# Performance work log

Hardware: AMD Instinct MI355X
Metric: run time of the kernel (lower is better)

Reference implementation:

```python
import jax, jax.numpy as jnp
import numpy as np

NU = 500000   # num_users
NI = 500000   # num_items
E = 128       # embedding_dim
F = 172       # feature_dim
B = 65536     # number of events in the batch
MSG = 2 * E + F  # GRU input dim = 428


def _gru_cell(x, h, wih, whh, bih, bhh):
    # PyTorch GRUCell: gates ordered (r, z, n)
    gi = x @ wih.T + bih            # [B, 3E]
    gh = h @ whh.T + bhh            # [B, 3E]
    ir, iz, in_ = jnp.split(gi, 3, axis=-1)
    hr, hz, hn = jnp.split(gh, 3, axis=-1)
    r = jax.nn.sigmoid(ir + hr)
    z = jax.nn.sigmoid(iz + hz)
    n = jnp.tanh(in_ + r * hn)
    return (1.0 - z) * n + z * h


def setup_inputs() -> dict:
    key = jax.random.key(0)
    ks = jax.random.split(key, 18)
    s = 0.05  # init scale ~ 1/sqrt(E)
    return {
        "user_ids": jax.random.randint(ks[0], (B,), 0, NU),
        "item_ids": jax.random.randint(ks[1], (B,), 0, NI),
        "timestamps": jax.random.uniform(ks[2], (B,), dtype=jnp.float32) * 1000.0,
        "features": jax.random.normal(ks[3], (B, F), dtype=jnp.float32),
        "query_time": 1200,
        "memory": jax.random.normal(ks[4], (NU + NI, E), dtype=jnp.float32) * 0.1,
        "last_time": jax.random.uniform(ks[5], (NU + NI,), dtype=jnp.float32) * 1000.0,
        "time_w": jax.random.normal(ks[6], (E,), dtype=jnp.float32) * 0.01,  # Linear(1,E,bias=False)
        "u_wih": jax.random.normal(ks[7], (3 * E, MSG), dtype=jnp.float32) * s,
        "u_whh": jax.random.normal(ks[8], (3 * E, E), dtype=jnp.float32) * s,
        "u_bih": jax.random.normal(ks[9], (3 * E,), dtype=jnp.float32) * s,
        "u_bhh": jax.random.normal(ks[10], (3 * E,), dtype=jnp.float32) * s,
        "i_wih": jax.random.normal(ks[11], (3 * E, MSG), dtype=jnp.float32) * s,
        "i_whh": jax.random.normal(ks[12], (3 * E, E), dtype=jnp.float32) * s,
        "i_bih": jax.random.normal(ks[13], (3 * E,), dtype=jnp.float32) * s,
        "i_bhh": jax.random.normal(ks[14], (3 * E,), dtype=jnp.float32) * s,
        "gate_w": jax.random.normal(ks[15], (E, 2 * E), dtype=jnp.float32) * s,
        "gate_b": jnp.zeros((E,), dtype=jnp.float32),
        "pred_w": jax.random.normal(ks[16], (E, E), dtype=jnp.float32) * s,
        "pred_b": jnp.zeros((E,), dtype=jnp.float32),
    }


def reference(user_ids, item_ids, timestamps, features, query_time, memory, last_time,
              time_w, u_wih, u_whh, u_bih, u_bhh, i_wih, i_whh, i_bih, i_bhh,
              gate_w, gate_b, pred_w, pred_b):
    item_nodes = item_ids + NU  # offset items into global node id space
    # per-event gather from node memory
    old_user = memory[user_ids]          # [B, E]
    old_item = memory[item_nodes]        # [B, E]
    last_u = last_time[user_ids]         # [B]
    last_i = last_time[item_nodes]       # [B]

    du = (timestamps - last_u)[:, None]  # [B, 1]
    di = (timestamps - last_i)[:, None]
    # time projection: emb * (1 + Linear(dt))
    proj_user = old_user * (1.0 + du * time_w)
    proj_item = old_item * (1.0 + di * time_w)

    d_query = (jnp.float32(query_time) - last_u)[:, None]
    query_user = old_user * (1.0 + d_query * time_w)

    # peer message mode: user_msg = proj_item, item_msg = proj_user
    user_input = jnp.concatenate([proj_user, proj_item, features], axis=-1)  # [B, MSG]
    item_input = jnp.concatenate([proj_item, proj_user, features], axis=-1)

    new_user = _gru_cell(user_input, old_user, u_wih, u_whh, u_bih, u_bhh)
    new_item = _gru_cell(item_input, old_item, i_wih, i_whh, i_bih, i_bhh)

    # memory gate: g*new + (1-g)*old
    gu = jax.nn.sigmoid(jnp.concatenate([old_user, new_user], axis=-1) @ gate_w.T + gate_b)
    gi = jax.nn.sigmoid(jnp.concatenate([old_item, new_item], axis=-1) @ gate_w.T + gate_b)
    new_user = gu * new_user + (1.0 - gu) * old_user
    new_item = gi * new_item + (1.0 - gi) * old_item

    pred_item_emb = query_user @ pred_w.T + pred_b
    return (pred_item_emb, new_user, new_item)
```

## Files before the change

kernel.cpp:

```cpp
#include <hip/hip_runtime.h>
#include <cstdint>
#include <cstddef>

#define CNU 500000
#define CB  65536
#define CE  128
#define CF  172
#define EV  64

typedef unsigned short ushort_t;
typedef __attribute__((ext_vector_type(8))) short b8;
typedef __attribute__((ext_vector_type(4))) short b4;
typedef __attribute__((ext_vector_type(4))) float f4;

#define MFMA16(a,b,c) __builtin_amdgcn_mfma_f32_16x16x32_bf16((a),(b),(c),0,0,0)

#define FRAG 512
#define U_KT 18
#define U_NT 24
#define U_SZ (U_NT*U_KT*FRAG)
#define PU_OFF 0
#define PI_OFF U_SZ
#define PG_OFF (2*U_SZ)
#define G_SZ (8*8*FRAG)
#define PP_OFF (PG_OFF + G_SZ)
#define P_SZ (8*4*FRAG)

#define SWZ(r, c) ((c) ^ (((r) & 7) << 3))
#define AFRAG(T, r, c) (*(const b8*)&(T)[(r)][SWZ((r), (c))])

__device__ __forceinline__ ushort_t f2bf(float f) {
  unsigned u = __float_as_uint(f);
  return (ushort_t)((u + 0x7FFFu + ((u >> 16) & 1u)) >> 16);
}
__device__ __forceinline__ float bf2f(ushort_t h) {
  return __uint_as_float(((unsigned)h) << 16);
}
__device__ __forceinline__ float sigmoid_(float x) { return 1.0f/(1.0f+__expf(-x)); }
__device__ __forceinline__ float tanh_(float x) { float e=__expf(2.0f*x); return 1.0f-2.0f/(e+1.0f); }

struct __align__(16) SLds {
  ushort_t PU[EV][128];
  ushort_t PI[EV][128];
  ushort_t FE[EV][192];
  ushort_t OU[EV][128];
  ushort_t OI[EV][128];
  ushort_t QU[EV][128];
};

extern "C" __global__ void prep_weights(
    const float* __restrict__ u_wih, const float* __restrict__ u_whh,
    const float* __restrict__ i_wih, const float* __restrict__ i_whh,
    const float* __restrict__ gate_w, const float* __restrict__ pred_w,
    ushort_t* __restrict__ ws)
{
  const int stride = gridDim.x * blockDim.x;
  const int tid = blockIdx.x * blockDim.x + threadIdx.x;
  for (int i = tid; i < U_SZ; i += stride) {
    const int nt = i / (U_KT*FRAG);
    const int r1 = i - nt*(U_KT*FRAG);
    const int kt = r1 / FRAG;
    const int e  = r1 - kt*FRAG;
    const int l  = e >> 3, j = e & 7;
    const int n  = nt*16 + (l & 15);
    const int k  = (l >> 4)*8 + j;
    float vu, vi;
    if (kt < 14) {
      const int kk = kt*32 + k;
      vu = (kk < 428) ? u_wih[(size_t)n*428 + kk] : 0.0f;
      vi = (kk < 428) ? i_wih[(size_t)n*428 + kk] : 0.0f;
    } else {
      const int kk = (kt - 14)*32 + k;
      vu = u_whh[(size_t)n*128 + kk];
      vi = i_whh[(size_t)n*128 + kk];
    }
    ws[PU_OFF + i] = f2bf(vu);
    ws[PI_OFF + i] = f2bf(vi);
  }
  for (int i = tid; i < G_SZ; i += stride) {
    const int nt = i / (8*FRAG);
    const int r1 = i - nt*(8*FRAG);
    const int kt = r1 / FRAG;
    const int e  = r1 - kt*FRAG;
    const int l  = e >> 3, j = e & 7;
    const int n  = nt*16 + (l & 15);
    const int kk = kt*32 + (l >> 4)*8 + j;
    ws[PG_OFF + i] = f2bf(gate_w[(size_t)n*256 + kk]);
  }
  for (int i = tid; i < P_SZ; i += stride) {
    const int nt = i / (4*FRAG);
    const int r1 = i - nt*(4*FRAG);
    const int kt = r1 / FRAG;
    const int e  = r1 - kt*FRAG;
    const int l  = e >> 3, j = e & 7;
    const int n  = nt*16 + (l & 15);
    const int kk = kt*32 + (l >> 4)*8 + j;
    ws[PP_OFF + i] = f2bf(pred_w[(size_t)n*128 + kk]);
  }
}

extern "C" __global__ void __launch_bounds__(512, 2)
jodie_main(const int* __restrict__ user_ids, const int* __restrict__ item_ids,
           const float* __restrict__ timestamps, const float* __restrict__ features,
           const int* __restrict__ query_time, const float* __restrict__ memv,
           const float* __restrict__ last_time, const float* __restrict__ time_w,
           const float* __restrict__ u_bih, const float* __restrict__ u_bhh,
           const float* __restrict__ i_bih, const float* __restrict__ i_bhh,
           const float* __restrict__ gate_b, const float* __restrict__ pred_b,
           const ushort_t* __restrict__ ws, float* __restrict__ d_out)
{
  __shared__ SLds s;
  const int t  = threadIdx.x;
  const int e0 = blockIdx.x * EV;

  {
    const int c8 = (t & 15) * 8;
    const float qt = (float)query_time[0];
    const float4 tw0 = *(const float4*)&time_w[c8];
    const float4 tw1 = *(const float4*)&time_w[c8 + 4];
    const float twv[8] = {tw0.x,tw0.y,tw0.z,tw0.w, tw1.x,tw1.y,tw1.z,tw1.w};
#pragma unroll
    for (int ep = 0; ep < 2; ++ep) {
      const int e  = ep*32 + (t >> 4);
      const int ge = e0 + e;
      const int u   = user_ids[ge];
      const int itn = item_ids[ge] + CNU;
      const float ts = timestamps[ge];
      const float lu = last_time[u];
      const float li = last_time[itn];
      const float du = ts - lu, di = ts - li, dq = qt - lu;

      const float4 ou0 = *(const float4*)&memv[(size_t)u  *CE + c8];
      const float4 ou1 = *(const float4*)&memv[(size_t)u  *CE + c8 + 4];
      const float4 oi0 = *(const float4*)&memv[(size_t)itn*CE + c8];
      const float4 oi1 = *(const float4*)&memv[(size_t)itn*CE + c8 + 4];
      const float ouv[8] = {ou0.x,ou0.y,ou0.z,ou0.w, ou1.x,ou1.y,ou1.z,ou1.w};
      const float oiv[8] = {oi0.x,oi0.y,oi0.z,oi0.w, oi1.x,oi1.y,oi1.z,oi1.w};

      union { ushort_t u[8]; b8 v; } xu, xi, hu, hi, qv;
#pragma unroll
      for (int j = 0; j < 8; ++j) {
        xu.u[j] = f2bf(ouv[j] * (1.0f + du*twv[j]));
        xi.u[j] = f2bf(oiv[j] * (1.0f + di*twv[j]));
        hu.u[j] = f2bf(ouv[j]);
        hi.u[j] = f2bf(oiv[j]);
        qv.u[j] = f2bf(ouv[j] * (1.0f + dq*twv[j]));
      }
      *(b8*)&s.PU[e][SWZ(e, c8)] = xu.v;
      *(b8*)&s.PI[e][SWZ(e, c8)] = xi.v;
      *(b8*)&s.OU[e][SWZ(e, c8)] = hu.v;
      *(b8*)&s.OI[e][SWZ(e, c8)] = hi.v;
      *(b8*)&s.QU[e][SWZ(e, c8)] = qv.v;
    }
  }
  for (int i = t; i < EV*43; i += 512) {
    const int e = i / 43, q = i - e*43;
    const float4 fv = *(const float4*)&features[(size_t)(e0 + e)*CF + q*4];
    union { ushort_t u[4]; b4 v; } fb;
    fb.u[0] = f2bf(fv.x); fb.u[1] = f2bf(fv.y);
    fb.u[2] = f2bf(fv.z); fb.u[3] = f2bf(fv.w);
    *(b4*)&s.FE[e][SWZ(e, q*4)] = fb.v;
  }
  for (int i = t; i < EV*20; i += 512) {
    const int e = i / 20, c = 172 + (i - e*20);
    s.FE[e][SWZ(e, c)] = 0;
  }
  __syncthreads();

  const int wv   = t >> 6, l = t & 63;
  const int lrow = l & 15;
  const int lk   = (l >> 4) * 8;
  const int col  = wv*16 + lrow;

  {
    const float bp = pred_b[col];
    f4 ap[4];
#pragma unroll
    for (int m = 0; m < 4; ++m) ap[m] = (f4){bp,bp,bp,bp};
    const ushort_t* WP = ws + PP_OFF + (size_t)wv*4*FRAG + l*8;
#pragma unroll
    for (int kt = 0; kt < 4; ++kt) {
      b8 fp = *(const b8*)(WP + (size_t)kt*FRAG);
#pragma unroll
      for (int m = 0; m < 4; ++m) {
        b8 a = AFRAG(s.QU, m*16 + lrow, 32*kt + lk);
        ap[m] = MFMA16(a, fp, ap[m]);
      }
    }
#pragma unroll
    for (int m = 0; m < 4; ++m)
#pragma unroll
      for (int r4 = 0; r4 < 4; ++r4) {
        const int row = m*16 + (l >> 4)*4 + r4;
        d_out[(size_t)(e0 + row)*CE + col] = ap[m][r4];
      }
  }
  __syncthreads();

  const float bru = u_bih[col]     + u_bhh[col];
  const float bzu = u_bih[col+128] + u_bhh[col+128];
  const float bnu = u_bih[col+256];
  const float bhu = u_bhh[col+256];
  const float bri = i_bih[col]     + i_bhh[col];
  const float bzi = i_bih[col+128] + i_bhh[col+128];
  const float bni = i_bih[col+256];
  const float bhi = i_bhh[col+256];

  f4 aru[4], azu[4], anu[4], ari[4], azi[4], ani[4];
#pragma unroll
  for (int m = 0; m < 4; ++m) {
    aru[m] = (f4){bru,bru,bru,bru};  azu[m] = (f4){bzu,bzu,bzu,bzu};
    anu[m] = (f4){bnu,bnu,bnu,bnu};  ari[m] = (f4){bri,bri,bri,bri};
    azi[m] = (f4){bzi,bzi,bzi,bzi};  ani[m] = (f4){bni,bni,bni,bni};
  }

  const ushort_t* Wru = ws + PU_OFF + (size_t)(wv     )*U_KT*FRAG + l*8;
  const ushort_t* Wzu = ws + PU_OFF + (size_t)(wv +  8)*U_KT*FRAG + l*8;
  const ushort_t* Wnu = ws + PU_OFF + (size_t)(wv + 16)*U_KT*FRAG + l*8;
  const ushort_t* Wri = ws + PI_OFF + (size_t)(wv     )*U_KT*FRAG + l*8;
  const ushort_t* Wzi = ws + PI_OFF + (size_t)(wv +  8)*U_KT*FRAG + l*8;
  const ushort_t* Wni = ws + PI_OFF + (size_t)(wv + 16)*U_KT*FRAG + l*8;

#define GI_STEP(TILE, pf, ktu, kti)                                          \
  {                                                                          \
    b8 a_[4];                                                                \
    _Pragma("unroll")                                                        \
    for (int m = 0; m < 4; ++m) a_[m] = AFRAG(TILE, m*16 + lrow, 32*(pf) + lk); \
    b8 fru = *(const b8*)(Wru + (size_t)(ktu)*FRAG);                         \
    b8 fzu = *(const b8*)(Wzu + (size_t)(ktu)*FRAG);                         \
    b8 fnu = *(const b8*)(Wnu + (size_t)(ktu)*FRAG);                         \
    b8 fri = *(const b8*)(Wri + (size_t)(kti)*FRAG);                         \
    b8 fzi = *(const b8*)(Wzi + (size_t)(kti)*FRAG);                         \
    b8 fni = *(const b8*)(Wni + (size_t)(kti)*FRAG);                         \
    _Pragma("unroll")                                                        \
    for (int m = 0; m < 4; ++m) {                                            \
      aru[m] = MFMA16(a_[m], fru, aru[m]);                                   \
      azu[m] = MFMA16(a_[m], fzu, azu[m]);                                   \
      anu[m] = MFMA16(a_[m], fnu, anu[m]);                                   \
      ari[m] = MFMA16(a_[m], fri, ari[m]);                                   \
      azi[m] = MFMA16(a_[m], fzi, azi[m]);                                   \
      ani[m] = MFMA16(a_[m], fni, ani[m]);                                   \
    }                                                                        \
  }

#pragma unroll
  for (int pf = 0; pf < 4; ++pf) GI_STEP(s.PU, pf, pf, pf + 4)
#pragma unroll
  for (int pf = 0; pf < 4; ++pf) GI_STEP(s.PI, pf, pf + 4, pf)
#pragma unroll
  for (int pf = 0; pf < 6; ++pf) GI_STEP(s.FE, pf, pf + 8, pf + 8)
#undef GI_STEP

  {
    f4 ah[4];
#pragma unroll
    for (int m = 0; m < 4; ++m) ah[m] = (f4){bhu,bhu,bhu,bhu};
#pragma unroll
    for (int kt = 0; kt < 4; ++kt) {
      b8 fr = *(const b8*)(Wru + (size_t)(14+kt)*FRAG);
      b8 fz = *(const b8*)(Wzu + (size_t)(14+kt)*FRAG);
      b8 fn = *(const b8*)(Wnu + (size_t)(14+kt)*FRAG);
#pragma unroll
      for (int m = 0; m < 4; ++m) {
        b8 h = AFRAG(s.OU, m*16 + lrow, 32*kt + lk);
        aru[m] = MFMA16(h, fr, aru[m]);
        azu[m] = MFMA16(h, fz, azu[m]);
        ah[m]  = MFMA16(h, fn, ah[m]);
      }
    }
#pragma unroll
    for (int m = 0; m < 4; ++m)
#pragma unroll
      for (int r4 = 0; r4 < 4; ++r4) {
        const int row = m*16 + (l >> 4)*4 + r4;
        const float rr = sigmoid_(aru[m][r4]);
        const float zz = sigmoid_(azu[m][r4]);
        const float nn = tanh_(anu[m][r4] + rr*ah[m][r4]);
        const float h  = bf2f(s.OU[row][SWZ(row, col)]);
        s.QU[row][SWZ(row, col)] = f2bf((1.0f - zz)*nn + zz*h);
      }
  }
  __syncthreads();

  {
    f4 ah[4];
#pragma unroll
    for (int m = 0; m < 4; ++m) ah[m] = (f4){bhi,bhi,bhi,bhi};
#pragma unroll
    for (int kt = 0; kt < 4; ++kt) {
      b8 fr = *(const b8*)(Wri + (size_t)(14+kt)*FRAG);
      b8 fz = *(const b8*)(Wzi + (size_t)(14+kt)*FRAG);
      b8 fn = *(const b8*)(Wni + (size_t)(14+kt)*FRAG);
#pragma unroll
      for (int m = 0; m < 4; ++m) {
        b8 h = AFRAG(s.OI, m*16 + lrow, 32*kt + lk);
        ari[m] = MFMA16(h, fr, ari[m]);
        azi[m] = MFMA16(h, fz, azi[m]);
        ah[m]  = MFMA16(h, fn, ah[m]);
      }
    }
#pragma unroll
    for (int m = 0; m < 4; ++m)
#pragma unroll
      for (int r4 = 0; r4 < 4; ++r4) {
        const int row = m*16 + (l >> 4)*4 + r4;
        const float rr = sigmoid_(ari[m][r4]);
        const float zz = sigmoid_(azi[m][r4]);
        const float nn = tanh_(ani[m][r4] + rr*ah[m][r4]);
        const float h  = bf2f(s.OI[row][SWZ(row, col)]);
        s.PU[row][SWZ(row, col)] = f2bf((1.0f - zz)*nn + zz*h);
      }
  }
  __syncthreads();

  {
    const float gb = gate_b[col];
    f4 agu[4], agi[4];
#pragma unroll
    for (int m = 0; m < 4; ++m) { agu[m] = (f4){gb,gb,gb,gb}; agi[m] = agu[m]; }
    const ushort_t* WG = ws + PG_OFF + (size_t)wv*8*FRAG + l*8;
#pragma unroll
    for (int kt = 0; kt < 8; ++kt) {
      b8 fg = *(const b8*)(WG + (size_t)kt*FRAG);
#pragma unroll
      for (int m = 0; m < 4; ++m) {
        b8 au = (kt < 4) ? AFRAG(s.OU, m*16 + lrow, 32*kt + lk)
                         : AFRAG(s.QU, m*16 + lrow, 32*(kt-4) + lk);
        b8 ai = (kt < 4) ? AFRAG(s.OI, m*16 + lrow, 32*kt + lk)
                         : AFRAG(s.PU, m*16 + lrow, 32*(kt-4) + lk);
        agu[m] = MFMA16(au, fg, agu[m]);
        agi[m] = MFMA16(ai, fg, agi[m]);
      }
    }
    float* __restrict__ outu = d_out + (size_t)CB*CE;
    float* __restrict__ outi = d_out + (size_t)2*CB*CE;
#pragma unroll
    for (int m = 0; m < 4; ++m)
#pragma unroll
      for (int r4 = 0; r4 < 4; ++r4) {
        const int row = m*16 + (l >> 4)*4 + r4;
        const float gu = sigmoid_(agu[m][r4]);
        const float gi = sigmoid_(agi[m][r4]);
        const float hu  = bf2f(s.OU[row][SWZ(row, col)]);
        const float hpu = bf2f(s.QU[row][SWZ(row, col)]);
        const float hi  = bf2f(s.OI[row][SWZ(row, col)]);
        const float hpi = bf2f(s.PU[row][SWZ(row, col)]);
        outu[(size_t)(e0 + row)*CE + col] = gu*hpu + (1.0f - gu)*hu;
        outi[(size_t)(e0 + row)*CE + col] = gi*hpi + (1.0f - gi)*hi;
      }
  }
}

extern "C" void kernel_launch(void* const* d_in, const int* in_sizes, int n_in,
                              void* d_out, int out_size, void* d_ws, size_t ws_size,
                              hipStream_t stream) {
  const int*   user_ids   = (const int*)d_in[0];
  const int*   item_ids   = (const int*)d_in[1];
  const float* timestamps = (const float*)d_in[2];
  const float* features   = (const float*)d_in[3];
  const int*   query_time = (const int*)d_in[4];
  const float* memv       = (const float*)d_in[5];
  const float* last_time  = (const float*)d_in[6];
  const float* time_w     = (const float*)d_in[7];
  const float* u_wih = (const float*)d_in[8];
  const float* u_whh = (const float*)d_in[9];
  const float* u_bih = (const float*)d_in[10];
  const float* u_bhh = (const float*)d_in[11];
  const float* i_wih = (const float*)d_in[12];
  const float* i_whh = (const float*)d_in[13];
  const float* i_bih = (const float*)d_in[14];
  const float* i_bhh = (const float*)d_in[15];
  const float* gate_w = (const float*)d_in[16];
  const float* gate_b = (const float*)d_in[17];
  const float* pred_w = (const float*)d_in[18];
  const float* pred_b = (const float*)d_in[19];
  ushort_t* ws = (ushort_t*)d_ws;
  float* out = (float*)d_out;

  prep_weights<<<dim3(256), dim3(256), 0, stream>>>(u_wih, u_whh, i_wih, i_whh,
                                                    gate_w, pred_w, ws);
  jodie_main<<<dim3(CB/EV), dim3(512), 0, stream>>>(user_ids, item_ids, timestamps,
                                                    features, query_time, memv,
                                                    last_time, time_w,
                                                    u_bih, u_bhh, i_bih, i_bhh,
                                                    gate_b, pred_b, ws, out);
}
```

Baseline: 140.1 us.

## Split user and item GRU across two wave groups in 1024-thread blocks

Doubles the block to 1024 threads and assigns user-side and item-side GRU/gate work to separate groups of 8 waves, so each wave keeps 4 accumulator sets instead of 6. This roughly halves per-wave serial MFMA work and register pressure, and also removes one barrier phase. The gather loop is flattened to one event per thread and bf16 conversion uses packed intrinsics. Risks include higher register pressure under launch_bounds(1024,4), fewer resident blocks, and the pred GEMM running only on group 0, which leaves group 1 idle during it.

```diff
diff --git a/kernel.cpp b/kernel.cpp
--- a/kernel.cpp
+++ b/kernel.cpp
@@ -1,4 +1,5 @@
 #include <hip/hip_runtime.h>
+#include <hip/hip_bf16.h>
 #include <cstdint>
 #include <cstddef>
 
@@ -29,6 +30,10 @@
 #define SWZ(r, c) ((c) ^ (((r) & 7) << 3))
 #define AFRAG(T, r, c) (*(const b8*)&(T)[(r)][SWZ((r), (c))])
 
+__device__ __forceinline__ unsigned pk2bf(float a, float b) {
+  __hip_bfloat162 h = __float22bfloat162_rn(make_float2(a, b));
+  return *reinterpret_cast<unsigned*>(&h);
+}
 __device__ __forceinline__ ushort_t f2bf(float f) {
   unsigned u = __float_as_uint(f);
   return (ushort_t)((u + 0x7FFFu + ((u >> 16) & 1u)) >> 16);
@@ -99,7 +104,7 @@
   }
 }
 
-extern "C" __global__ void __launch_bounds__(512, 2)
+extern "C" __global__ void __launch_bounds__(1024, 4)
 jodie_main(const int* __restrict__ user_ids, const int* __restrict__ item_ids,
            const float* __restrict__ timestamps, const float* __restrict__ features,
            const int* __restrict__ query_time, const float* __restrict__ memv,
@@ -115,64 +120,73 @@
 
   {
     const int c8 = (t & 15) * 8;
+    const int e  = t >> 4;
+    const int ge = e0 + e;
     const float qt = (float)query_time[0];
     const float4 tw0 = *(const float4*)&time_w[c8];
     const float4 tw1 = *(const float4*)&time_w[c8 + 4];
     const float twv[8] = {tw0.x,tw0.y,tw0.z,tw0.w, tw1.x,tw1.y,tw1.z,tw1.w};
-#pragma unroll
-    for (int ep = 0; ep < 2; ++ep) {
-      const int e  = ep*32 + (t >> 4);
-      const int ge = e0 + e;
-      const int u   = user_ids[ge];
-      const int itn = item_ids[ge] + CNU;
-      const float ts = timestamps[ge];
-      const float lu = last_time[u];
-      const float li = last_time[itn];
-      const float du = ts - lu, di = ts - li, dq = qt - lu;
-
-      const float4 ou0 = *(const float4*)&memv[(size_t)u  *CE + c8];
-      const float4 ou1 = *(const float4*)&memv[(size_t)u  *CE + c8 + 4];
-      const float4 oi0 = *(const float4*)&memv[(size_t)itn*CE + c8];
-      const float4 oi1 = *(const float4*)&memv[(size_t)itn*CE + c8 + 4];
-      const float ouv[8] = {ou0.x,ou0.y,ou0.z,ou0.w, ou1.x,ou1.y,ou1.z,ou1.w};
-      const float oiv[8] = {oi0.x,oi0.y,oi0.z,oi0.w, oi1.x,oi1.y,oi1.z,oi1.w};
-
-      union { ushort_t u[8]; b8 v; } xu, xi, hu, hi, qv;
-#pragma unroll
-      for (int j = 0; j < 8; ++j) {
-        xu.u[j] = f2bf(ouv[j] * (1.0f + du*twv[j]));
-        xi.u[j] = f2bf(oiv[j] * (1.0f + di*twv[j]));
-        hu.u[j] = f2bf(ouv[j]);
-        hi.u[j] = f2bf(oiv[j]);
-        qv.u[j] = f2bf(ouv[j] * (1.0f + dq*twv[j]));
-      }
-      *(b8*)&s.PU[e][SWZ(e, c8)] = xu.v;
-      *(b8*)&s.PI[e][SWZ(e, c8)] = xi.v;
-      *(b8*)&s.OU[e][SWZ(e, c8)] = hu.v;
-      *(b8*)&s.OI[e][SWZ(e, c8)] = hi.v;
-      *(b8*)&s.QU[e][SWZ(e, c8)] = qv.v;
-    }
-  }
-  for (int i = t; i < EV*43; i += 512) {
+
+    const int u   = user_ids[ge];
+    const int itn = item_ids[ge] + CNU;
+    const float ts = timestamps[ge];
+    const float lu = last_time[u];
+    const float li = last_time[itn];
+    const float du = ts - lu, di = ts - li, dq = qt - lu;
+
+    const float4 ou0 = *(const float4*)&memv[(size_t)u  *CE + c8];
+    const float4 ou1 = *(const float4*)&memv[(size_t)u  *CE + c8 + 4];
+    const float4 oi0 = *(const float4*)&memv[(size_t)itn*CE + c8];
+    const float4 oi1 = *(const float4*)&memv[(size_t)itn*CE + c8 + 4];
+    const float ouv[8] = {ou0.x,ou0.y,ou0.z,ou0.w, ou1.x,ou1.y,ou1.z,ou1.w};
+    const float oiv[8] = {oi0.x,oi0.y,oi0.z,oi0.w, oi1.x,oi1.y,oi1.z,oi1.w};
+
+    union U8 { unsigned q[4]; b8 v; };
+    U8 xu, xi, hu, hi, qv;
+#pragma unroll
+    for (int j = 0; j < 8; j += 2) {
+      xu.q[j>>1] = pk2bf(ouv[j]*(1.0f + du*twv[j]), ouv[j+1]*(1.0f + du*twv[j+1]));
+      xi.q[j>>1] = pk2bf(oiv[j]*(1.0f + di*twv[j]), oiv[j+1]*(1.0f + di*twv[j+1]));
+      hu.q[j>>1] = pk2bf(ouv[j], ouv[j+1]);
+      hi.q[j>>1] = pk2bf(oiv[j], oiv[j+1]);
+      qv.q[j>>1] = pk2bf(ouv[j]*(1.0f + dq*twv[j]), ouv[j+1]*(1.0f + dq*twv[j+1]));
+    }
+    *(b8*)&s.PU[e][SWZ(e, c8)] = xu.v;
+    *(b8*)&s.PI[e][SWZ(e, c8)] = xi.v;
+    *(b8*)&s.OU[e][SWZ(e, c8)] = hu.v;
+    *(b8*)&s.OI[e][SWZ(e, c8)] = hi.v;
+    *(b8*)&s.QU[e][SWZ(e, c8)] = qv.v;
+  }
+  for (int i = t; i < EV*43; i += 1024) {
     const int e = i / 43, q = i - e*43;
     const float4 fv = *(const float4*)&features[(size_t)(e0 + e)*CF + q*4];
-    union { ushort_t u[4]; b4 v; } fb;
-    fb.u[0] = f2bf(fv.x); fb.u[1] = f2bf(fv.y);
-    fb.u[2] = f2bf(fv.z); fb.u[3] = f2bf(fv.w);
+    union { unsigned q[2]; b4 v; } fb;
+    fb.q[0] = pk2bf(fv.x, fv.y);
+    fb.q[1] = pk2bf(fv.z, fv.w);
     *(b4*)&s.FE[e][SWZ(e, q*4)] = fb.v;
   }
-  for (int i = t; i < EV*20; i += 512) {
+  for (int i = t; i < EV*20; i += 1024) {
     const int e = i / 20, c = 172 + (i - e*20);
     s.FE[e][SWZ(e, c)] = 0;
   }
   __syncthreads();
 
-  const int wv   = t >> 6, l = t & 63;
+  const int w    = t >> 6;
+  const int g    = w >> 3;
+  const int wv   = w & 7;
+  const int l    = t & 63;
   const int lrow = l & 15;
   const int lk   = (l >> 4) * 8;
   const int col  = wv*16 + lrow;
 
-  {
+  const float* bih = g ? i_bih : u_bih;
+  const float* bhh = g ? i_bhh : u_bhh;
+  const ushort_t* WB = ws + (g ? PI_OFF : PU_OFF);
+  const ushort_t* Wr = WB + (size_t)(wv     )*U_KT*FRAG + l*8;
+  const ushort_t* Wz = WB + (size_t)(wv +  8)*U_KT*FRAG + l*8;
+  const ushort_t* Wn = WB + (size_t)(wv + 16)*U_KT*FRAG + l*8;
+
+  if (g == 0) {
     const float bp = pred_b[col];
     f4 ap[4];
 #pragma unroll
@@ -195,158 +209,109 @@
         d_out[(size_t)(e0 + row)*CE + col] = ap[m][r4];
       }
   }
+
+  const float br = bih[col]     + bhh[col];
+  const float bz = bih[col+128] + bhh[col+128];
+  const float bn = bih[col+256];
+  const float bh = bhh[col+256];
+  f4 ar[4], az[4], an[4], ah[4];
+#pragma unroll
+  for (int m = 0; m < 4; ++m) {
+    ar[m] = (f4){br,br,br,br};
+    az[m] = (f4){bz,bz,bz,bz};
+    an[m] = (f4){bn,bn,bn,bn};
+    ah[m] = (f4){bh,bh,bh,bh};
+  }
+
+#pragma unroll
+  for (int pf = 0; pf < 14; ++pf) {
+    b8 a_[4];
+    if (pf < 8) {
+      const ushort_t (*A)[128] = ((pf < 4) ^ g) ? s.PU : s.PI;
+      const int c = 32*(pf & 3);
+#pragma unroll
+      for (int m = 0; m < 4; ++m) a_[m] = AFRAG(A, m*16 + lrow, c + lk);
+    } else {
+      const int c = 32*(pf - 8);
+#pragma unroll
+      for (int m = 0; m < 4; ++m) a_[m] = AFRAG(s.FE, m*16 + lrow, c + lk);
+    }
+    b8 fr = *(const b8*)(Wr + (size_t)pf*FRAG);
+    b8 fz = *(const b8*)(Wz + (size_t)pf*FRAG);
+    b8 fn = *(const b8*)(Wn + (size_t)pf*FRAG);
+#pragma unroll
+    for (int m = 0; m < 4; ++m) {
+      ar[m] = MFMA16(a_[m], fr, ar[m]);
+      az[m] = MFMA16(a_[m], fz, az[m]);
+      an[m] = MFMA16(a_[m], fn, an[m]);
+    }
+  }
+
+  {
+    const ushort_t (*H)[128] = g ? s.OI : s.OU;
+#pragma unroll
+    for (int kt = 0; kt < 4; ++kt) {
+      b8 fr = *(const b8*)(Wr + (size_t)(14+kt)*FRAG);
+      b8 fz = *(const b8*)(Wz + (size_t)(14+kt)*FRAG);
+      b8 fn = *(const b8*)(Wn + (size_t)(14+kt)*FRAG);
+#pragma unroll
+      for (int m = 0; m < 4; ++m) {
+        b8 h = AFRAG(H, m*16 + lrow, 32*kt + lk);
+        ar[m] = MFMA16(h, fr, ar[m]);
+        az[m] = MFMA16(h, fz, az[m]);
+        ah[m] = MFMA16(h, fn, ah[m]);
+      }
+    }
+  }
   __syncthreads();
 
-  const float bru = u_bih[col]     + u_bhh[col];
-  const float bzu = u_bih[col+128] + u_bhh[col+128];
-  const float bnu = u_bih[col+256];
-  const float bhu = u_bhh[col+256];
-  const float bri = i_bih[col]     + i_bhh[col];
-  const float bzi = i_bih[col+128] + i_bhh[col+128];
-  const float bni = i_bih[col+256];
-  const float bhi = i_bhh[col+256];
-
-  f4 aru[4], azu[4], anu[4], ari[4], azi[4], ani[4];
-#pragma unroll
-  for (int m = 0; m < 4; ++m) {
-    aru[m] = (f4){bru,bru,bru,bru};  azu[m] = (f4){bzu,bzu,bzu,bzu};
-    anu[m] = (f4){bnu,bnu,bnu,bnu};  ari[m] = (f4){bri,bri,bri,bri};
-    azi[m] = (f4){bzi,bzi,bzi,bzi};  ani[m] = (f4){bni,bni,bni,bni};
-  }
-
-  const ushort_t* Wru = ws + PU_OFF + (size_t)(wv     )*U_KT*FRAG + l*8;
-  const ushort_t* Wzu = ws + PU_OFF + (size_t)(wv +  8)*U_KT*FRAG + l*8;
-  const ushort_t* Wnu = ws + PU_OFF + (size_t)(wv + 16)*U_KT*FRAG + l*8;
-  const ushort_t* Wri = ws + PI_OFF + (size_t)(wv     )*U_KT*FRAG + l*8;
-  const ushort_t* Wzi = ws + PI_OFF + (size_t)(wv +  8)*U_KT*FRAG + l*8;
-  const ushort_t* Wni = ws + PI_OFF + (size_t)(wv + 16)*U_KT*FRAG + l*8;
-
-#define GI_STEP(TILE, pf, ktu, kti)                                          \
-  {                                                                          \
-    b8 a_[4];                                                                \
-    _Pragma("unroll")                                                        \
-    for (int m = 0; m < 4; ++m) a_[m] = AFRAG(TILE, m*16 + lrow, 32*(pf) + lk); \
-    b8 fru = *(const b8*)(Wru + (size_t)(ktu)*FRAG);                         \
-    b8 fzu = *(const b8*)(Wzu + (size_t)(ktu)*FRAG);                         \
-    b8 fnu = *(const b8*)(Wnu + (size_t)(ktu)*FRAG);                         \
-    b8 fri = *(const b8*)(Wri + (size_t)(kti)*FRAG);                         \
-    b8 fzi = *(const b8*)(Wzi + (size_t)(kti)*FRAG);                         \
-    b8 fni = *(const b8*)(Wni + (size_t)(kti)*FRAG);                         \
-    _Pragma("unroll")                                                        \
-    for (int m = 0; m < 4; ++m) {                                            \
-      aru[m] = MFMA16(a_[m], fru, aru[m]);                                   \
-      azu[m] = MFMA16(a_[m], fzu, azu[m]);                                   \
-      anu[m] = MFMA16(a_[m], fnu, anu[m]);                                   \
-      ari[m] = MFMA16(a_[m], fri, ari[m]);                                   \
-      azi[m] = MFMA16(a_[m], fzi, azi[m]);                                   \
-      ani[m] = MFMA16(a_[m], fni, ani[m]);                                   \
-    }                                                                        \
-  }
-
-#pragma unroll
-  for (int pf = 0; pf < 4; ++pf) GI_STEP(s.PU, pf, pf, pf + 4)
-#pragma unroll
-  for (int pf = 0; pf < 4; ++pf) GI_STEP(s.PI, pf, pf + 4, pf)
-#pragma unroll
-  for (int pf = 0; pf < 6; ++pf) GI_STEP(s.FE, pf, pf + 8, pf + 8)
-#undef GI_STEP
-
+  float hv[16], hpv[16];
   {
-    f4 ah[4];
-#pragma unroll
-    for (int m = 0; m < 4; ++m) ah[m] = (f4){bhu,bhu,bhu,bhu};
-#pragma unroll
-    for (int kt = 0; kt < 4; ++kt) {
-      b8 fr = *(const b8*)(Wru + (size_t)(14+kt)*FRAG);
-      b8 fz = *(const b8*)(Wzu + (size_t)(14+kt)*FRAG);
-      b8 fn = *(const b8*)(Wnu + (size_t)(14+kt)*FRAG);
-#pragma unroll
-      for (int m = 0; m < 4; ++m) {
-        b8 h = AFRAG(s.OU, m*16 + lrow, 32*kt + lk);
-        aru[m] = MFMA16(h, fr, aru[m]);
-        azu[m] = MFMA16(h, fz, azu[m]);
-        ah[m]  = MFMA16(h, fn, ah[m]);
-      }
-    }
+    ushort_t (*DST)[128] = g ? s.PU : s.QU;
+    const ushort_t (*H)[128] = g ? s.OI : s.OU;
 #pragma unroll
     for (int m = 0; m < 4; ++m)
 #pragma unroll
       for (int r4 = 0; r4 < 4; ++r4) {
         const int row = m*16 + (l >> 4)*4 + r4;
-        const float rr = sigmoid_(aru[m][r4]);
-        const float zz = sigmoid_(azu[m][r4]);
-        const float nn = tanh_(anu[m][r4] + rr*ah[m][r4]);
-        const float h  = bf2f(s.OU[row][SWZ(row, col)]);
-        s.QU[row][SWZ(row, col)] = f2bf((1.0f - zz)*nn + zz*h);
+        const float rr = sigmoid_(ar[m][r4]);
+        const float zz = sigmoid_(az[m][r4]);
+        const float nn = tanh_(an[m][r4] + rr*ah[m][r4]);
+        const float h  = bf2f(H[row][SWZ(row, col)]);
+        const float hp = (1.0f - zz)*nn + zz*h;
+        hv [m*4 + r4] = h;
+        hpv[m*4 + r4] = hp;
+        DST[row][SWZ(row, col)] = f2bf(hp);
       }
   }
   __syncthreads();
 
   {
-    f4 ah[4];
-#pragma unroll
-    for (int m = 0; m < 4; ++m) ah[m] = (f4){bhi,bhi,bhi,bhi};
-#pragma unroll
-    for (int kt = 0; kt < 4; ++kt) {
-      b8 fr = *(const b8*)(Wri + (size_t)(14+kt)*FRAG);
-      b8 fz = *(const b8*)(Wzi + (size_t)(14+kt)*FRAG);
-      b8 fn = *(const b8*)(Wni + (size_t)(14+kt)*FRAG);
+    const float gb = gate_b[col];
+    f4 ag[4];
+#pragma unroll
+    for (int m = 0; m < 4; ++m) ag[m] = (f4){gb,gb,gb,gb};
+    const ushort_t* WG = ws + PG_OFF + (size_t)wv*8*FRAG + l*8;
+    const ushort_t (*HO)[128] = g ? s.OI : s.OU;
+    const ushort_t (*HN)[128] = g ? s.PU : s.QU;
+#pragma unroll
+    for (int kt = 0; kt < 8; ++kt) {
+      b8 fg = *(const b8*)(WG + (size_t)kt*FRAG);
 #pragma unroll
       for (int m = 0; m < 4; ++m) {
-        b8 h = AFRAG(s.OI, m*16 + lrow, 32*kt + lk);
-        ari[m] = MFMA16(h, fr, ari[m]);
-        azi[m] = MFMA16(h, fz, azi[m]);
-        ah[m]  = MFMA16(h, fn, ah[m]);
-      }
-    }
+        b8 a = (kt < 4) ? AFRAG(HO, m*16 + lrow, 32*kt + lk)
+                        : AFRAG(HN, m*16 + lrow, 32*(kt-4) + lk);
+        ag[m] = MFMA16(a, fg, ag[m]);
+      }
+    }
+    float* __restrict__ outp = d_out + (size_t)(1 + g)*CB*CE;
 #pragma unroll
     for (int m = 0; m < 4; ++m)
 #pragma unroll
       for (int r4 = 0; r4 < 4; ++r4) {
         const int row = m*16 + (l >> 4)*4 + r4;
-        const float rr = sigmoid_(ari[m][r4]);
-        const float zz = sigmoid_(azi[m][r4]);
-        const float nn = tanh_(ani[m][r4] + rr*ah[m][r4]);
-        const float h  = bf2f(s.OI[row][SWZ(row, col)]);
-        s.PU[row][SWZ(row, col)] = f2bf((1.0f - zz)*nn + zz*h);
-      }
-  }
-  __syncthreads();
-
-  {
-    const float gb = gate_b[col];
-    f4 agu[4], agi[4];
-#pragma unroll
-    for (int m = 0; m < 4; ++m) { agu[m] = (f4){gb,gb,gb,gb}; agi[m] = agu[m]; }
-    const ushort_t* WG = ws + PG_OFF + (size_t)wv*8*FRAG + l*8;
-#pragma unroll
-    for (int kt = 0; kt < 8; ++kt) {
-      b8 fg = *(const b8*)(WG + (size_t)kt*FRAG);
-#pragma unroll
-      for (int m = 0; m < 4; ++m) {
-        b8 au = (kt < 4) ? AFRAG(s.OU, m*16 + lrow, 32*kt + lk)
-                         : AFRAG(s.QU, m*16 + lrow, 32*(kt-4) + lk);
-        b8 ai = (kt < 4) ? AFRAG(s.OI, m*16 + lrow, 32*kt + lk)
-                         : AFRAG(s.PU, m*16 + lrow, 32*(kt-4) + lk);
-        agu[m] = MFMA16(au, fg, agu[m]);
-        agi[m] = MFMA16(ai, fg, agi[m]);
-      }
-    }
-    float* __restrict__ outu = d_out + (size_t)CB*CE;
-    float* __restrict__ outi = d_out + (size_t)2*CB*CE;
-#pragma unroll
-    for (int m = 0; m < 4; ++m)
-#pragma unroll
-      for (int r4 = 0; r4 < 4; ++r4) {
-        const int row = m*16 + (l >> 4)*4 + r4;
-        const float gu = sigmoid_(agu[m][r4]);
-        const float gi = sigmoid_(agi[m][r4]);
-        const float hu  = bf2f(s.OU[row][SWZ(row, col)]);
-        const float hpu = bf2f(s.QU[row][SWZ(row, col)]);
-        const float hi  = bf2f(s.OI[row][SWZ(row, col)]);
-        const float hpi = bf2f(s.PU[row][SWZ(row, col)]);
-        outu[(size_t)(e0 + row)*CE + col] = gu*hpu + (1.0f - gu)*hu;
-        outi[(size_t)(e0 + row)*CE + col] = gi*hpi + (1.0f - gi)*hi;
+        const float gg = sigmoid_(ag[m][r4]);
+        outp[(size_t)(e0 + row)*CE + col] = gg*hpv[m*4 + r4] + (1.0f - gg)*hv[m*4 + r4];
       }
   }
 }
@@ -379,9 +344,9 @@
 
   prep_weights<<<dim3(256), dim3(256), 0, stream>>>(u_wih, u_whh, i_wih, i_whh,
                                                     gate_w, pred_w, ws);
-  jodie_main<<<dim3(CB/EV), dim3(512), 0, stream>>>(user_ids, item_ids, timestamps,
-                                                    features, query_time, memv,
-                                                    last_time, time_w,
-                                                    u_bih, u_bhh, i_bih, i_bhh,
-                                                    gate_b, pred_b, ws, out);
-}
+  jodie_main<<<dim3(CB/EV), dim3(1024), 0, stream>>>(user_ids, item_ids, timestamps,
+                                                     features, query_time, memv,
+                                                     last_time, time_w,
+                                                     u_bih, u_bhh, i_bih, i_bhh,
+                                                     gate_b, pred_b, ws, out);
+}
```

Result: slower. 160.8 us (+14.8%).
